# Kernel tuning notes

Hardware: AMD Instinct MI355X
Metric: run time of the kernel (lower is better)

## Reference

```python
import jax, jax.numpy as jnp
import numpy as np

N = 100000      # nodes
E = 600000      # directed edges (before self-loops)
NFEAT = 128
NHID = 128
NCLASS = 64


def setup_inputs() -> dict:
    key = jax.random.key(0)
    k1, k2, k3, k4 = jax.random.split(key, 4)
    x = jax.random.normal(k1, (N, NFEAT), dtype=jnp.float32)
    edge_index = jax.random.randint(k2, (2, E), 0, N, dtype=jnp.int32)
    # GCNConv learned params (Glorot-ish init), bias zeros as in PyG default
    W1 = jax.random.normal(k3, (NFEAT, NHID), dtype=jnp.float32) / jnp.sqrt(NFEAT)
    b1 = jnp.zeros((NHID,), dtype=jnp.float32)
    W2 = jax.random.normal(k4, (NHID, NCLASS), dtype=jnp.float32) / jnp.sqrt(NHID)
    b2 = jnp.zeros((NCLASS,), dtype=jnp.float32)
    return {"x": x, "edge_index": edge_index, "W1": W1, "b1": b1, "W2": W2, "b2": b2}


def _gcn_layer(x, src, dst, norm, W, b, n):
    # PyG GCNConv: linear transform, then normalized neighbor aggregation, then bias
    h = x @ W                                   # [N, out]
    msg = h[src] * norm[:, None]                # [E+N, out] gather + scale
    agg = jax.ops.segment_sum(msg, dst, num_segments=n)  # scatter-add
    return agg + b


def reference(x, edge_index, W1, b1, W2, b2):
    n = x.shape[0]
    # add self-loops (PyG gcn_norm default add_self_loops=True)
    loops = jnp.arange(n, dtype=edge_index.dtype)
    src = jnp.concatenate([edge_index[0], loops])
    dst = jnp.concatenate([edge_index[1], loops])
    # symmetric normalization: D^-1/2 (A+I) D^-1/2
    deg = jax.ops.segment_sum(jnp.ones_like(dst, dtype=x.dtype), dst, num_segments=n)
    d_inv_sqrt = jnp.where(deg > 0, jax.lax.rsqrt(deg), 0.0)
    norm = d_inv_sqrt[src] * d_inv_sqrt[dst]
    h = jax.nn.relu(_gcn_layer(x, src, dst, norm, W1, b1, n))
    # F.dropout with training=False is identity -> omitted in eval reference
    return _gcn_layer(h, src, dst, norm, W2, b2, n)
```

## Files before the change

kernel.cpp:

```cpp
#include <hip/hip_runtime.h>


typedef unsigned short u16;
typedef unsigned int u32;
typedef __attribute__((ext_vector_type(8))) short bf16x8;
typedef __attribute__((ext_vector_type(4))) float f32x4;

#define BSH 9
#define BMSK ((1 << BSH) - 1)
#define MAXBK 256
#define SEG 2560
#define HISTB 128
#define GEMMB 1024

__device__ __forceinline__ u16 f2b(float f) {
  u32 u = __float_as_uint(f);
  u32 r = (u + 0x7FFFu + ((u >> 16) & 1u)) >> 16;
  return (u16)r;
}
__device__ __forceinline__ u32 pk2(float a, float b) {
  return (u32)f2b(a) | ((u32)f2b(b) << 16);
}
__device__ __forceinline__ void dec8(uint4 v, float f[8]) {
  f[0] = __uint_as_float(v.x << 16);
  f[1] = __uint_as_float(v.x & 0xFFFF0000u);
  f[2] = __uint_as_float(v.y << 16);
  f[3] = __uint_as_float(v.y & 0xFFFF0000u);
  f[4] = __uint_as_float(v.z << 16);
  f[5] = __uint_as_float(v.z & 0xFFFF0000u);
  f[6] = __uint_as_float(v.w << 16);
  f[7] = __uint_as_float(v.w & 0xFFFF0000u);
}
__device__ __forceinline__ void fma8(uint4 v, float d, float acc[8]) {
  acc[0] = fmaf(__uint_as_float(v.x << 16), d, acc[0]);
  acc[1] = fmaf(__uint_as_float(v.x & 0xFFFF0000u), d, acc[1]);
  acc[2] = fmaf(__uint_as_float(v.y << 16), d, acc[2]);
  acc[3] = fmaf(__uint_as_float(v.y & 0xFFFF0000u), d, acc[3]);
  acc[4] = fmaf(__uint_as_float(v.z << 16), d, acc[4]);
  acc[5] = fmaf(__uint_as_float(v.z & 0xFFFF0000u), d, acc[5]);
  acc[6] = fmaf(__uint_as_float(v.w << 16), d, acc[6]);
  acc[7] = fmaf(__uint_as_float(v.w & 0xFFFF0000u), d, acc[7]);
}


__global__ __launch_bounds__(256) void prep_hist_k(const void* __restrict__ W1,
                                                   const void* __restrict__ b1,
                                                   const void* __restrict__ W2,
                                                   const void* __restrict__ b2,
                                                   u16* __restrict__ W1t, u16* __restrict__ ob1,
                                                   u16* __restrict__ W2t, u16* __restrict__ ob2,
                                                   int* __restrict__ mode,
                                                   const int* __restrict__ dst,
                                                   int* __restrict__ bhist,
                                                   int E, int PREPB) {
  const int tid = threadIdx.x;

  if ((int)blockIdx.x >= PREPB) {
    __shared__ int lh[MAXBK];
    const int hb = (int)blockIdx.x - PREPB;
    for (int j = tid; j < MAXBK; j += 256) lh[j] = 0;
    __syncthreads();
    const int chunk = (E + HISTB - 1) / HISTB;
    const int e0 = hb * chunk;
    const int e1 = min(E, e0 + chunk);
    for (int e = e0 + tid; e < e1; e += 256) atomicAdd(&lh[dst[e] >> BSH], 1);
    __syncthreads();
    for (int j = tid; j < MAXBK; j += 256) {
      int v = lh[j];
      if (v) atomicAdd(&bhist[j], v);
    }
    return;
  }

  __shared__ int cnt_s;
  if (tid == 0) cnt_s = 0;
  __syncthreads();
  int c = 0;
  for (int j = tid; j < 4096; j += 256) {
    u32 e = (((const u16*)W1)[j] >> 7) & 0xFFu;
    if (e >= 100u && e <= 130u) c++;
  }
  atomicAdd(&cnt_s, c);
  __syncthreads();
  const int m = (cnt_s < 3328) ? 1 : 0;
  if (blockIdx.x == 0 && tid == 0) *mode = m;

  int i = blockIdx.x * 256 + tid;
  if (i < 24768) {
    int j = i;
    const void* src;
    u16* dstp;
    int sidx, didx;
    if (j < 16384) {
      int nn = j >> 7, k = j & 127;
      src = W1; dstp = W1t; sidx = k * 128 + nn; didx = j;
    } else if ((j -= 16384) < 128) {
      src = b1; dstp = ob1; sidx = j; didx = j;
    } else if ((j -= 128) < 8192) {
      int nn = j >> 7, k = j & 127;
      src = W2; dstp = W2t; sidx = k * 64 + nn; didx = j;
    } else {
      j -= 8192;
      src = b2; dstp = ob2; sidx = j; didx = j;
    }
    dstp[didx] = m ? f2b(((const float*)src)[sidx]) : ((const u16*)src)[sidx];
  }
}


__global__ __launch_bounds__(256) void part_k(const int* __restrict__ src,
                                              const int* __restrict__ dst,
                                              const int* __restrict__ bhist,
                                              int* __restrict__ boff,
                                              int2* __restrict__ tmp,
                                              int E, int NBK) {
  __shared__ int ls[SEG];
  __shared__ int ld_[SEG];
  __shared__ int lh[MAXBK];
  __shared__ int base_[MAXBK];
  __shared__ int bsl[MAXBK];
  const int tid = threadIdx.x;

  int ov = (tid < NBK) ? bhist[tid] : 0;
  bsl[tid] = ov;
  __syncthreads();
#pragma unroll
  for (int off = 1; off < 256; off <<= 1) {
    int add = (tid >= off) ? bsl[tid - off] : 0;
    __syncthreads();
    bsl[tid] += add;
    __syncthreads();
  }
  bsl[tid] -= ov;
  if (tid < MAXBK) lh[tid] = 0;
  __syncthreads();

  const int e0 = blockIdx.x * SEG;
  const int len = min(SEG, E - e0);
  for (int j = tid; j < len; j += 256) {
    int s = src[e0 + j];
    int d = dst[e0 + j];
    ls[j] = s;
    ld_[j] = d;
    atomicAdd(&lh[d >> BSH], 1);
  }
  __syncthreads();
  if (tid < NBK) {
    int hh = lh[tid];
    base_[tid] = hh ? bsl[tid] + atomicAdd(&boff[tid], hh) : 0;
    lh[tid] = 0;
  }
  __syncthreads();
  for (int j = tid; j < len; j += 256) {
    int d = ld_[j];
    int bk = d >> BSH;
    int r = atomicAdd(&lh[bk], 1);
    tmp[base_[bk] + r] = make_int2(ls[j], d);
  }
}


__global__ __launch_bounds__(256) void nbgemm_k(const int2* __restrict__ tmp,
                                                const int* __restrict__ bhist,
                                                float* __restrict__ dinv,
                                                int4* __restrict__ ninfo,
                                                int* __restrict__ spI,
                                                int np, int NBK,
                                                const void* __restrict__ Araw,
                                                const u16* __restrict__ Wt,
                                                u16* __restrict__ hout, int M,
                                                const int* __restrict__ mode) {
  __shared__ int bsl[MAXBK];
  __shared__ int cntl[1 << BSH];
  __shared__ int curl[1 << BSH];
  __shared__ int sc2[256];
  const int tid = threadIdx.x;

  if ((int)blockIdx.x < NBK) {
    const int b = blockIdx.x;

    int ov = (tid < NBK) ? bhist[tid] : 0;
    bsl[tid] = ov;
    __syncthreads();
#pragma unroll
    for (int off = 1; off < 256; off <<= 1) {
      int add = (tid >= off) ? bsl[tid - off] : 0;
      __syncthreads();
      bsl[tid] += add;
      __syncthreads();
    }
    bsl[tid] -= ov;
    cntl[tid] = 0;
    cntl[tid + 256] = 0;
    curl[tid] = 0;
    curl[tid + 256] = 0;
    __syncthreads();

    const int bs = bsl[b];
    const int be = bs + bhist[b];
    const int lo = b << BSH;

    for (int e = bs + tid; e < be; e += 256) {
      int2 p = tmp[e];
      atomicAdd(&cntl[p.y & BMSK], 1);
    }
    __syncthreads();

    const int c0 = cntl[2 * tid];
    const int c1 = cntl[2 * tid + 1];
    const int s2 = c0 + c1;
    sc2[tid] = s2;
    __syncthreads();
#pragma unroll
    for (int off = 1; off < 256; off <<= 1) {
      int add = (tid >= off) ? sc2[tid - off] : 0;
      __syncthreads();
      sc2[tid] += add;
      __syncthreads();
    }
    const int excl = sc2[tid] - s2;
    const int e0n = excl;
    const int e1n = excl + c0;

    {
      int i0 = lo + 2 * tid;
      if (i0 < np) {
        float dv = rsqrtf((float)c0 + 1.0f);
        dinv[i0] = dv;
        ninfo[i0] = make_int4(bs + e0n, c0, __float_as_int(dv), 0);
      }
      int i1 = i0 + 1;
      if (i1 < np) {
        float dv = rsqrtf((float)c1 + 1.0f);
        dinv[i1] = dv;
        ninfo[i1] = make_int4(bs + e1n, c1, __float_as_int(dv), 0);
      }
    }
    cntl[2 * tid] = e0n;
    cntl[2 * tid + 1] = e1n;
    __syncthreads();

    for (int e = bs + tid; e < be; e += 256) {
      int2 p = tmp[e];
      int loc = p.y & BMSK;
      int r = atomicAdd(&curl[loc], 1);
      spI[bs + cntl[loc] + r] = p.x;
    }
    return;
  }

  const int mcv = *mode;
  const int wv = tid >> 6, lane = tid & 63, lr = lane & 15, lq = lane >> 4;
  const int ntiles = (M + 63) >> 6;

  for (int t = (int)blockIdx.x - NBK; t < ntiles; t += GEMMB) {
    const int r0 = t * 64;
    const int arow = r0 + wv * 16 + lr;
    const bool rok = (arow < M);

    bf16x8 a[4];
    if (mcv) {
      const float* xr = (const float*)Araw + (size_t)arow * 128 + lq * 8;
#pragma unroll
      for (int s = 0; s < 4; ++s) {
        uint4 u = make_uint4(0u, 0u, 0u, 0u);
        if (rok) {
          float4 f0 = *(const float4*)(xr + s * 32);
          float4 f1 = *(const float4*)(xr + s * 32 + 4);
          u.x = pk2(f0.x, f0.y);
          u.y = pk2(f0.z, f0.w);
          u.z = pk2(f1.x, f1.y);
          u.w = pk2(f1.z, f1.w);
        }
        a[s] = *(const bf16x8*)&u;
      }
    } else {
      const u16* xr = (const u16*)Araw + (size_t)arow * 128 + lq * 8;
#pragma unroll
      for (int s = 0; s < 4; ++s) {
        uint4 u = rok ? *(const uint4*)(xr + s * 32) : make_uint4(0u, 0u, 0u, 0u);
        a[s] = *(const bf16x8*)&u;
      }
    }

#pragma unroll
    for (int nt = 0; nt < 8; ++nt) {
      f32x4 acc = {0.f, 0.f, 0.f, 0.f};
#pragma unroll
      for (int s = 0; s < 4; ++s) {
        bf16x8 b = *(const bf16x8*)&Wt[(size_t)(nt * 16 + lr) * 128 + s * 32 + lq * 8];
        acc = __builtin_amdgcn_mfma_f32_16x16x32_bf16(a[s], b, acc, 0, 0, 0);
      }
#pragma unroll
      for (int r = 0; r < 4; ++r) {
        int row = r0 + wv * 16 + lq * 4 + r;
        if (row < M) hout[(size_t)row * 128 + nt * 16 + lr] = f2b(acc[r]);
      }
    }
  }
}


__global__ __launch_bounds__(256) void fusedB_k(const u16* __restrict__ h,
                                                const int* __restrict__ spI,
                                                const int4* __restrict__ ninfo,
                                                const float* __restrict__ dinv,
                                                const u16* __restrict__ b1,
                                                const u16* __restrict__ W2t,
                                                u16* __restrict__ g, int n) {
  __shared__ __align__(16) u16 As[16 * 136];
  const int tid = threadIdx.x, wv = tid >> 6, lane = tid & 63;
  const int lq = lane >> 4, lr = lane & 15;
  const int base = blockIdx.x * 16;
  const int i = base + wv * 4 + lq;
  const bool valid = (i < n);

  int start = 0, c = 0;
  float di = 0.f;
  if (valid) {
    int4 ni = ninfo[i];
    start = ni.x;
    c = ni.y;
    di = __int_as_float(ni.z);
  }
  float acc[8];
  {
    uint4 v = valid ? *(const uint4*)(h + (size_t)i * 128 + lr * 8)
                    : make_uint4(0u, 0u, 0u, 0u);
    float f[8];
    dec8(v, f);
#pragma unroll
    for (int j = 0; j < 8; ++j) acc[j] = f[j] * di;
  }
  const int bl = lq * 16;
  for (int bs = 0; __any(bs < c); bs += 16) {
    int m = c - bs;
    m = m < 0 ? 0 : (m > 16 ? 16 : m);
    int s = 0;
    float dv = 0.f;
    if (lr < m) {
      s = spI[start + bs + lr];
      dv = dinv[s];
    }
    int mmw = m;
    mmw = max(mmw, __shfl_xor(mmw, 16));
    mmw = max(mmw, __shfl_xor(mmw, 32));
    for (int e = 0; e < mmw; e += 4) {
      int s0 = __shfl(s, bl + e), s1 = __shfl(s, bl + e + 1);
      int s2 = __shfl(s, bl + e + 2), s3 = __shfl(s, bl + e + 3);
      float d0 = __shfl(dv, bl + e);
      float d1 = __shfl(dv, bl + e + 1);
      float d2 = __shfl(dv, bl + e + 2);
      float d3 = __shfl(dv, bl + e + 3);
      uint4 v0 = *(const uint4*)(h + (size_t)s0 * 128 + lr * 8);
      uint4 v1 = *(const uint4*)(h + (size_t)s1 * 128 + lr * 8);
      uint4 v2 = *(const uint4*)(h + (size_t)s2 * 128 + lr * 8);
      uint4 v3 = *(const uint4*)(h + (size_t)s3 * 128 + lr * 8);
      fma8(v0, d0, acc);
      fma8(v1, d1, acc);
      fma8(v2, d2, acc);
      fma8(v3, d3, acc);
    }
  }
  {
    uint4 bv = *(const uint4*)(b1 + lr * 8);
    float bf[8];
    dec8(bv, bf);
    float o[8];
#pragma unroll
    for (int j = 0; j < 8; ++j) o[j] = fmaxf(fmaf(acc[j], di, bf[j]), 0.f);
    uint4 ov;
    ov.x = pk2(o[0], o[1]);
    ov.y = pk2(o[2], o[3]);
    ov.z = pk2(o[4], o[5]);
    ov.w = pk2(o[6], o[7]);
    *(uint4*)&As[(wv * 4 + lq) * 136 + lr * 8] = ov;
  }
  __syncthreads();

  bf16x8 a[4];
#pragma unroll
  for (int s = 0; s < 4; ++s)
    a[s] = *(const bf16x8*)&As[lr * 136 + s * 32 + lq * 8];
  {
    const int nt = wv;
    f32x4 acc4 = {0.f, 0.f, 0.f, 0.f};
#pragma unroll
    for (int s = 0; s < 4; ++s) {
      bf16x8 b = *(const bf16x8*)&W2t[(nt * 16 + lr) * 128 + s * 32 + lq * 8];
      acc4 = __builtin_amdgcn_mfma_f32_16x16x32_bf16(a[s], b, acc4, 0, 0, 0);
    }
#pragma unroll
    for (int r = 0; r < 4; ++r) {
      int row = base + lq * 4 + r;
      if (row < n) g[(size_t)row * 64 + nt * 16 + lr] = f2b(acc4[r]);
    }
  }
}


__global__ __launch_bounds__(256) void agg2_k(const u16* __restrict__ g,
                                              const int* __restrict__ spI,
                                              const int4* __restrict__ ninfo,
                                              const float* __restrict__ dinv,
                                              const u16* __restrict__ b2,
                                              void* __restrict__ outv, int n,
                                              const int* __restrict__ mode) {
  const int lane = threadIdx.x & 63;
  const int o8 = lane >> 3, l8 = lane & 7;
  const int i = blockIdx.x * 32 + (threadIdx.x >> 6) * 8 + o8;
  const bool valid = (i < n);

  int start = 0, c = 0;
  float di = 0.f;
  if (valid) {
    int4 ni = ninfo[i];
    start = ni.x;
    c = ni.y;
    di = __int_as_float(ni.z);
  }
  float acc[8];
  {
    uint4 v = valid ? *(const uint4*)(g + (size_t)i * 64 + l8 * 8)
                    : make_uint4(0u, 0u, 0u, 0u);
    float f[8];
    dec8(v, f);
#pragma unroll
    for (int j = 0; j < 8; ++j) acc[j] = f[j] * di;
  }
  const int bl = o8 * 8;
  for (int base = 0; __any(base < c); base += 8) {
    int m = c - base;
    m = m < 0 ? 0 : (m > 8 ? 8 : m);
    int s = 0;
    float dv = 0.f;
    if (l8 < m) {
      s = spI[start + base + l8];
      dv = dinv[s];
    }
    int mmw = m;
    mmw = max(mmw, __shfl_xor(mmw, 8));
    mmw = max(mmw, __shfl_xor(mmw, 16));
    mmw = max(mmw, __shfl_xor(mmw, 32));
    for (int e = 0; e < mmw; e += 4) {
      int s0 = __shfl(s, bl + e), s1 = __shfl(s, bl + e + 1);
      int s2 = __shfl(s, bl + e + 2), s3 = __shfl(s, bl + e + 3);
      float d0 = __shfl(dv, bl + e);
      float d1 = __shfl(dv, bl + e + 1);
      float d2 = __shfl(dv, bl + e + 2);
      float d3 = __shfl(dv, bl + e + 3);
      uint4 v0 = *(const uint4*)(g + (size_t)s0 * 64 + l8 * 8);
      uint4 v1 = *(const uint4*)(g + (size_t)s1 * 64 + l8 * 8);
      uint4 v2 = *(const uint4*)(g + (size_t)s2 * 64 + l8 * 8);
      uint4 v3 = *(const uint4*)(g + (size_t)s3 * 64 + l8 * 8);
      fma8(v0, d0, acc);
      fma8(v1, d1, acc);
      fma8(v2, d2, acc);
      fma8(v3, d3, acc);
    }
  }
  if (valid) {
    uint4 bv = *(const uint4*)(b2 + l8 * 8);
    float bf[8];
    dec8(bv, bf);
    float o[8];
#pragma unroll
    for (int j = 0; j < 8; ++j) o[j] = fmaf(acc[j], di, bf[j]);
    if (*mode) {
      float* op = (float*)outv + (size_t)i * 64 + l8 * 8;
      *(float4*)op = make_float4(o[0], o[1], o[2], o[3]);
      *(float4*)(op + 4) = make_float4(o[4], o[5], o[6], o[7]);
    } else {
      uint4 ov;
      ov.x = pk2(o[0], o[1]);
      ov.y = pk2(o[2], o[3]);
      ov.z = pk2(o[4], o[5]);
      ov.w = pk2(o[6], o[7]);
      *(uint4*)((u16*)outv + (size_t)i * 64 + l8 * 8) = ov;
    }
  }
}


extern "C" void kernel_launch(void* const* d_in, const int* in_sizes, int n_in,
                              void* d_out, int out_size, void* d_ws, size_t ws_size,
                              hipStream_t stream) {
  const void* x_raw  = d_in[0];
  const int*  ei     = (const int*)d_in[1];
  const void* W1_raw = d_in[2];
  const void* b1_raw = d_in[3];
  const void* W2_raw = d_in[4];
  const void* b2_raw = d_in[5];

  const int N = in_sizes[0] / 128;
  const int E = in_sizes[1] / 2;
  const int NP = ((N + 255) / 256) * 256;
  const int NBK = (NP + (1 << BSH) - 1) >> BSH;
  const int PREPB = (24768 + 255) / 256;

  char* ws = (char*)d_ws;
  size_t off = 0;
  auto alloc = [&](size_t bytes) -> void* {
    void* p = ws + off;
    off = (off + bytes + 255) & ~(size_t)255;
    return p;
  };
  int*   mode    = (int*)alloc(4);
  int*   bz      = (int*)alloc((size_t)2 * MAXBK * 4);
  int*   bhist   = bz;
  int*   boff    = bz + MAXBK;
  float* dinv    = (float*)alloc((size_t)NP * 4);
  int4*  ninfo   = (int4*)alloc((size_t)NP * 16);
  int*   spI     = (int*)alloc((size_t)E * 4);
  int2*  tmp     = (int2*)alloc((size_t)E * 8);
  u16*   W1t     = (u16*)alloc((size_t)128 * 128 * 2);
  u16*   b1b     = (u16*)alloc(128 * 2);
  u16*   W2t     = (u16*)alloc((size_t)64 * 128 * 2);
  u16*   b2b     = (u16*)alloc(64 * 2);
  u16*   h       = (u16*)alloc((size_t)N * 128 * 2);
  u16*   g       = (u16*)alloc((size_t)N * 64 * 2);

  const int pb = (E + SEG - 1) / SEG;

  hipMemsetAsync(bz, 0, (size_t)2 * MAXBK * 4, stream);
  prep_hist_k<<<PREPB + HISTB, 256, 0, stream>>>(W1_raw, b1_raw, W2_raw, b2_raw,
                                                 W1t, b1b, W2t, b2b, mode,
                                                 ei + E, bhist, E, PREPB);
  part_k<<<pb, 256, 0, stream>>>(ei, ei + E, bhist, boff, tmp, E, NBK);
  nbgemm_k<<<NBK + GEMMB, 256, 0, stream>>>(tmp, bhist, dinv, ninfo, spI, NP, NBK,
                                            x_raw, W1t, h, N, mode);
  fusedB_k<<<(N + 15) / 16, 256, 0, stream>>>(h, spI, ninfo, dinv, b1b, W2t, g, N);
  agg2_k<<<(N + 31) / 32, 256, 0, stream>>>(g, spI, ninfo, dinv, b2b, d_out, N, mode);
}
```

Before: 203.8 us.

## Split neighbor build from GEMM1, prefetch A tiles, pre-swizzle W1 fragments

The fused neighbor-build plus GEMM kernel is split into two kernels. The first builds the CSR structure (degrees, offsets, neighbor indices). The second, gemm1_k, runs the first-layer GEMM with register double-buffering, loading the next tile's A rows before computing the current tile. W1 is rearranged during prep into an MFMA-fragment order, so each lane's B operand is one contiguous 16-byte load, and the GEMM grid is resized to 784 blocks. The split adds one kernel launch and removes the possible overlap between the two phases in exchange for simpler, better-pipelined GEMM code.

New measurement: 197.7 us. -3.0%, faster.

```diff
diff --git a/kernel.cpp b/kernel.cpp
--- a/kernel.cpp
+++ b/kernel.cpp
@@ -11,7 +11,7 @@
 #define MAXBK 256
 #define SEG 2560
 #define HISTB 128
-#define GEMMB 1024
+#define GEMMB 784
 
 __device__ __forceinline__ u16 f2b(float f) {
   u32 u = __float_as_uint(f);
@@ -47,7 +47,7 @@
                                                    const void* __restrict__ b1,
                                                    const void* __restrict__ W2,
                                                    const void* __restrict__ b2,
-                                                   u16* __restrict__ W1t, u16* __restrict__ ob1,
+                                                   u16* __restrict__ W1f, u16* __restrict__ ob1,
                                                    u16* __restrict__ W2t, u16* __restrict__ ob2,
                                                    int* __restrict__ mode,
                                                    const int* __restrict__ dst,
@@ -92,8 +92,10 @@
     u16* dstp;
     int sidx, didx;
     if (j < 16384) {
-      int nn = j >> 7, k = j & 127;
-      src = W1; dstp = W1t; sidx = k * 128 + nn; didx = j;
+      int jj = j & 7, ln = (j >> 3) & 63, s = (j >> 9) & 3, nt = j >> 11;
+      int k = s * 32 + (ln >> 4) * 8 + jj;
+      int nn = nt * 16 + (ln & 15);
+      src = W1; dstp = W1f; sidx = k * 128 + nn; didx = j;
     } else if ((j -= 16384) < 128) {
       src = b1; dstp = ob1; sidx = j; didx = j;
     } else if ((j -= 128) < 8192) {
@@ -160,136 +162,149 @@
 }
 
 
-__global__ __launch_bounds__(256) void nbgemm_k(const int2* __restrict__ tmp,
+__global__ __launch_bounds__(256) void nbuild_k(const int2* __restrict__ tmp,
                                                 const int* __restrict__ bhist,
                                                 float* __restrict__ dinv,
                                                 int4* __restrict__ ninfo,
                                                 int* __restrict__ spI,
-                                                int np, int NBK,
-                                                const void* __restrict__ Araw,
-                                                const u16* __restrict__ Wt,
-                                                u16* __restrict__ hout, int M,
-                                                const int* __restrict__ mode) {
+                                                int np, int NBK) {
   __shared__ int bsl[MAXBK];
   __shared__ int cntl[1 << BSH];
   __shared__ int curl[1 << BSH];
   __shared__ int sc2[256];
   const int tid = threadIdx.x;
-
-  if ((int)blockIdx.x < NBK) {
-    const int b = blockIdx.x;
-
-    int ov = (tid < NBK) ? bhist[tid] : 0;
-    bsl[tid] = ov;
-    __syncthreads();
-#pragma unroll
-    for (int off = 1; off < 256; off <<= 1) {
-      int add = (tid >= off) ? bsl[tid - off] : 0;
-      __syncthreads();
-      bsl[tid] += add;
-      __syncthreads();
-    }
-    bsl[tid] -= ov;
-    cntl[tid] = 0;
-    cntl[tid + 256] = 0;
-    curl[tid] = 0;
-    curl[tid + 256] = 0;
-    __syncthreads();
-
-    const int bs = bsl[b];
-    const int be = bs + bhist[b];
-    const int lo = b << BSH;
-
-    for (int e = bs + tid; e < be; e += 256) {
-      int2 p = tmp[e];
-      atomicAdd(&cntl[p.y & BMSK], 1);
-    }
-    __syncthreads();
-
-    const int c0 = cntl[2 * tid];
-    const int c1 = cntl[2 * tid + 1];
-    const int s2 = c0 + c1;
-    sc2[tid] = s2;
-    __syncthreads();
-#pragma unroll
-    for (int off = 1; off < 256; off <<= 1) {
-      int add = (tid >= off) ? sc2[tid - off] : 0;
-      __syncthreads();
-      sc2[tid] += add;
-      __syncthreads();
-    }
-    const int excl = sc2[tid] - s2;
-    const int e0n = excl;
-    const int e1n = excl + c0;
-
-    {
-      int i0 = lo + 2 * tid;
-      if (i0 < np) {
-        float dv = rsqrtf((float)c0 + 1.0f);
-        dinv[i0] = dv;
-        ninfo[i0] = make_int4(bs + e0n, c0, __float_as_int(dv), 0);
+  const int b = blockIdx.x;
+
+  int ov = (tid < NBK) ? bhist[tid] : 0;
+  bsl[tid] = ov;
+  __syncthreads();
+#pragma unroll
+  for (int off = 1; off < 256; off <<= 1) {
+    int add = (tid >= off) ? bsl[tid - off] : 0;
+    __syncthreads();
+    bsl[tid] += add;
+    __syncthreads();
+  }
+  bsl[tid] -= ov;
+  cntl[tid] = 0;
+  cntl[tid + 256] = 0;
+  curl[tid] = 0;
+  curl[tid + 256] = 0;
+  __syncthreads();
+
+  const int bs = bsl[b];
+  const int be = bs + bhist[b];
+  const int lo = b << BSH;
+
+  for (int e = bs + tid; e < be; e += 256) {
+    int2 p = tmp[e];
+    atomicAdd(&cntl[p.y & BMSK], 1);
+  }
+  __syncthreads();
+
+  const int c0 = cntl[2 * tid];
+  const int c1 = cntl[2 * tid + 1];
+  const int s2 = c0 + c1;
+  sc2[tid] = s2;
+  __syncthreads();
+#pragma unroll
+  for (int off = 1; off < 256; off <<= 1) {
+    int add = (tid >= off) ? sc2[tid - off] : 0;
+    __syncthreads();
+    sc2[tid] += add;
+    __syncthreads();
+  }
+  const int excl = sc2[tid] - s2;
+  const int e0n = excl;
+  const int e1n = excl + c0;
+
+  {
+    int i0 = lo + 2 * tid;
+    if (i0 < np) {
+      float dv = rsqrtf((float)c0 + 1.0f);
+      dinv[i0] = dv;
+      ninfo[i0] = make_int4(bs + e0n, c0, __float_as_int(dv), 0);
+    }
+    int i1 = i0 + 1;
+    if (i1 < np) {
+      float dv = rsqrtf((float)c1 + 1.0f);
+      dinv[i1] = dv;
+      ninfo[i1] = make_int4(bs + e1n, c1, __float_as_int(dv), 0);
+    }
+  }
+  cntl[2 * tid] = e0n;
+  cntl[2 * tid + 1] = e1n;
+  __syncthreads();
+
+  for (int e = bs + tid; e < be; e += 256) {
+    int2 p = tmp[e];
+    int loc = p.y & BMSK;
+    int r = atomicAdd(&curl[loc], 1);
+    spI[bs + cntl[loc] + r] = p.x;
+  }
+}
+
+
+__device__ __forceinline__ void loadA(const void* Araw, int arow, bool rok,
+                                      int lq, int mcv, bf16x8 a[4]) {
+  if (mcv) {
+    const float* xr = (const float*)Araw + (size_t)arow * 128 + lq * 8;
+#pragma unroll
+    for (int s = 0; s < 4; ++s) {
+      uint4 u = make_uint4(0u, 0u, 0u, 0u);
+      if (rok) {
+        float4 f0 = *(const float4*)(xr + s * 32);
+        float4 f1 = *(const float4*)(xr + s * 32 + 4);
+        u.x = pk2(f0.x, f0.y);
+        u.y = pk2(f0.z, f0.w);
+        u.z = pk2(f1.x, f1.y);
+        u.w = pk2(f1.z, f1.w);
       }
-      int i1 = i0 + 1;
-      if (i1 < np) {
-        float dv = rsqrtf((float)c1 + 1.0f);
-        dinv[i1] = dv;
-        ninfo[i1] = make_int4(bs + e1n, c1, __float_as_int(dv), 0);
-      }
-    }
-    cntl[2 * tid] = e0n;
-    cntl[2 * tid + 1] = e1n;
-    __syncthreads();
-
-    for (int e = bs + tid; e < be; e += 256) {
-      int2 p = tmp[e];
-      int loc = p.y & BMSK;
-      int r = atomicAdd(&curl[loc], 1);
-      spI[bs + cntl[loc] + r] = p.x;
-    }
-    return;
-  }
-
+      a[s] = *(const bf16x8*)&u;
+    }
+  } else {
+    const u16* xr = (const u16*)Araw + (size_t)arow * 128 + lq * 8;
+#pragma unroll
+    for (int s = 0; s < 4; ++s) {
+      uint4 u = rok ? *(const uint4*)(xr + s * 32) : make_uint4(0u, 0u, 0u, 0u);
+      a[s] = *(const bf16x8*)&u;
+    }
+  }
+}
+
+__global__ __launch_bounds__(256) void gemm1_k(const void* __restrict__ Araw,
+                                               const u16* __restrict__ W1f,
+                                               u16* __restrict__ hout, int M,
+                                               const int* __restrict__ mode) {
+  const int tid = threadIdx.x;
   const int mcv = *mode;
   const int wv = tid >> 6, lane = tid & 63, lr = lane & 15, lq = lane >> 4;
   const int ntiles = (M + 63) >> 6;
 
-  for (int t = (int)blockIdx.x - NBK; t < ntiles; t += GEMMB) {
+  int t = blockIdx.x;
+  if (t >= ntiles) return;
+
+  bf16x8 a_cur[4], a_nxt[4];
+  {
+    const int arow = t * 64 + wv * 16 + lr;
+    loadA(Araw, arow, arow < M, lq, mcv, a_cur);
+  }
+
+  for (; t < ntiles; t += GEMMB) {
+    const int tn = t + GEMMB;
+    if (tn < ntiles) {
+      const int arow = tn * 64 + wv * 16 + lr;
+      loadA(Araw, arow, arow < M, lq, mcv, a_nxt);
+    }
+
     const int r0 = t * 64;
-    const int arow = r0 + wv * 16 + lr;
-    const bool rok = (arow < M);
-
-    bf16x8 a[4];
-    if (mcv) {
-      const float* xr = (const float*)Araw + (size_t)arow * 128 + lq * 8;
-#pragma unroll
-      for (int s = 0; s < 4; ++s) {
-        uint4 u = make_uint4(0u, 0u, 0u, 0u);
-        if (rok) {
-          float4 f0 = *(const float4*)(xr + s * 32);
-          float4 f1 = *(const float4*)(xr + s * 32 + 4);
-          u.x = pk2(f0.x, f0.y);
-          u.y = pk2(f0.z, f0.w);
-          u.z = pk2(f1.x, f1.y);
-          u.w = pk2(f1.z, f1.w);
-        }
-        a[s] = *(const bf16x8*)&u;
-      }
-    } else {
-      const u16* xr = (const u16*)Araw + (size_t)arow * 128 + lq * 8;
-#pragma unroll
-      for (int s = 0; s < 4; ++s) {
-        uint4 u = rok ? *(const uint4*)(xr + s * 32) : make_uint4(0u, 0u, 0u, 0u);
-        a[s] = *(const bf16x8*)&u;
-      }
-    }
-
 #pragma unroll
     for (int nt = 0; nt < 8; ++nt) {
       f32x4 acc = {0.f, 0.f, 0.f, 0.f};
 #pragma unroll
       for (int s = 0; s < 4; ++s) {
-        bf16x8 b = *(const bf16x8*)&Wt[(size_t)(nt * 16 + lr) * 128 + s * 32 + lq * 8];
-        acc = __builtin_amdgcn_mfma_f32_16x16x32_bf16(a[s], b, acc, 0, 0, 0);
+        bf16x8 b = *(const bf16x8*)&W1f[(size_t)(((nt << 2) | s) << 6 | lane) * 8];
+        acc = __builtin_amdgcn_mfma_f32_16x16x32_bf16(a_cur[s], b, acc, 0, 0, 0);
       }
 #pragma unroll
       for (int r = 0; r < 4; ++r) {
@@ -297,6 +312,8 @@
         if (row < M) hout[(size_t)row * 128 + nt * 16 + lr] = f2b(acc[r]);
       }
     }
+#pragma unroll
+    for (int s = 0; s < 4; ++s) a_cur[s] = a_nxt[s];
   }
 }
 
@@ -513,7 +530,7 @@
   int4*  ninfo   = (int4*)alloc((size_t)NP * 16);
   int*   spI     = (int*)alloc((size_t)E * 4);
   int2*  tmp     = (int2*)alloc((size_t)E * 8);
-  u16*   W1t     = (u16*)alloc((size_t)128 * 128 * 2);
+  u16*   W1f     = (u16*)alloc((size_t)128 * 128 * 2);
   u16*   b1b     = (u16*)alloc(128 * 2);
   u16*   W2t     = (u16*)alloc((size_t)64 * 128 * 2);
   u16*   b2b     = (u16*)alloc(64 * 2);
@@ -524,11 +541,11 @@
 
   hipMemsetAsync(bz, 0, (size_t)2 * MAXBK * 4, stream);
   prep_hist_k<<<PREPB + HISTB, 256, 0, stream>>>(W1_raw, b1_raw, W2_raw, b2_raw,
-                                                 W1t, b1b, W2t, b2b, mode,
+                                                 W1f, b1b, W2t, b2b, mode,
                                                  ei + E, bhist, E, PREPB);
   part_k<<<pb, 256, 0, stream>>>(ei, ei + E, bhist, boff, tmp, E, NBK);
-  nbgemm_k<<<NBK + GEMMB, 256, 0, stream>>>(tmp, bhist, dinv, ninfo, spI, NP, NBK,
-                                            x_raw, W1t, h, N, mode);
+  nbuild_k<<<NBK, 256, 0, stream>>>(tmp, bhist, dinv, ninfo, spI, NP, NBK);
+  gemm1_k<<<GEMMB, 256, 0, stream>>>(x_raw, W1f, h, N, mode);
   fusedB_k<<<(N + 15) / 16, 256, 0, stream>>>(h, spI, ninfo, dinv, b1b, W2t, g, N);
   agg2_k<<<(N + 31) / 32, 256, 0, stream>>>(g, spI, ninfo, dinv, b2b, d_out, N, mode);
 }
```
